# Kernel tuning notes

Measured on AMD Instinct MI355X. Metric: run time of the kernel, lower is better.

## Reference

```python
import jax, jax.numpy as jnp
import numpy as np

PROMPT_LEN = 2048
VOCAB = 49408
DIM = 768


def setup_inputs() -> dict:
    key = jax.random.key(0)
    k1, k2 = jax.random.split(key)
    # prompt_embs initialized ~ N(0, 0.02) per nn.init.normal_(std=0.02)
    prompt_embs = jax.random.normal(k1, (PROMPT_LEN, DIM), dtype=jnp.float32) * 0.02
    # codebook (CLIP embedding table), fixed data (not a trainable param)
    clip_embs = jax.random.normal(k2, (VOCAB, DIM), dtype=jnp.float32)
    return {"prompt_embs": prompt_embs, "clip_embs": clip_embs}


def _find_nearest(prompt_embs, clip_embs):
    # torch.cdist with p=2 -> Euclidean distance. argmin is invariant under sqrt,
    # so we use the expanded squared-distance form (single GEMM + norms),
    # avoiding materializing the [P, D]-broadcast difference tensor.
    p_sq = jnp.sum(prompt_embs * prompt_embs, axis=-1, keepdims=True)  # [P, 1]
    c_sq = jnp.sum(clip_embs * clip_embs, axis=-1)                      # [V]
    cross = jnp.einsum("pd,vd->pv", prompt_embs, clip_embs)            # [P, V]
    d2 = p_sq + c_sq[None, :] - 2.0 * cross                             # [P, V]
    return jnp.argmin(d2, axis=1)                                       # [P]


def reference(prompt_embs, clip_embs):
    prompt_ids = _find_nearest(prompt_embs, clip_embs)      # [P] int
    vocab_embs = clip_embs[prompt_ids, :]                   # [P, D] gather
    # straight-through: value = vocab_embs, gradient flows to prompt_embs
    out_embs = jax.lax.stop_gradient(vocab_embs - prompt_embs) + prompt_embs
    return out_embs, prompt_ids
```

## Files before the change

### kernel.cpp

```cpp
#include <hip/hip_runtime.h>
#include <float.h>

#define PROMPT_LEN 2048
#define VOCAB 49408
#define DIM 768
#define ROWS_TOTAL (VOCAB + PROMPT_LEN)
#define NS 16
#define TM 64
#define TN 32
#define KC 64
#define KQ (KC / 4)
#define EPS 0.008f


__global__ void __launch_bounds__(1024) k_sumsq(const float* __restrict__ prompt,
                                                const float* __restrict__ clip,
                                                float* __restrict__ csq,
                                                unsigned* __restrict__ scal) {
    int tid  = threadIdx.x;
    int wid  = tid >> 6;
    int lane = tid & 63;
    int base = blockIdx.x * 128 + wid * 8;

    if (blockIdx.x == 0 && tid == 0) scal[0] = 0u;

    float locMin = FLT_MAX, locMax = 0.f;
    for (int r = base; r < base + 8; r += 2) {
        const float* s0 = (r     < VOCAB) ? clip + (size_t)r * DIM
                                          : prompt + (size_t)(r - VOCAB) * DIM;
        const float* s1 = (r + 1 < VOCAB) ? clip + (size_t)(r + 1) * DIM
                                          : prompt + (size_t)(r + 1 - VOCAB) * DIM;
        float4 a0 = ((const float4*)s0)[lane];
        float4 a1 = ((const float4*)s0)[64 + lane];
        float4 a2 = ((const float4*)s0)[128 + lane];
        float4 b0 = ((const float4*)s1)[lane];
        float4 b1 = ((const float4*)s1)[64 + lane];
        float4 b2 = ((const float4*)s1)[128 + lane];
        float sA = a0.x*a0.x + a0.y*a0.y + a0.z*a0.z + a0.w*a0.w
                 + a1.x*a1.x + a1.y*a1.y + a1.z*a1.z + a1.w*a1.w
                 + a2.x*a2.x + a2.y*a2.y + a2.z*a2.z + a2.w*a2.w;
        float sB = b0.x*b0.x + b0.y*b0.y + b0.z*b0.z + b0.w*b0.w
                 + b1.x*b1.x + b1.y*b1.y + b1.z*b1.z + b1.w*b1.w
                 + b2.x*b2.x + b2.y*b2.y + b2.z*b2.z + b2.w*b2.w;
        #pragma unroll
        for (int m = 32; m >= 1; m >>= 1) {
            sA += __shfl_xor(sA, m, 64);
            sB += __shfl_xor(sB, m, 64);
        }
        if (r < VOCAB)     locMin = fminf(locMin, sA); else locMax = fmaxf(locMax, sA);
        if (r + 1 < VOCAB) locMin = fminf(locMin, sB); else locMax = fmaxf(locMax, sB);
        if (lane == 0) {
            if (r < VOCAB)     csq[r] = sA;
            if (r + 1 < VOCAB) csq[r + 1] = sB;
        }
    }
    __shared__ float smn[16], smx[16];
    if (lane == 0) { smn[wid] = locMin; smx[wid] = locMax; }
    __syncthreads();
    if (tid == 0) {
        float mn = FLT_MAX, mx = 0.f;
        #pragma unroll
        for (int w = 0; w < 16; ++w) { mn = fminf(mn, smn[w]); mx = fmaxf(mx, smx[w]); }
        atomicMin(&scal[1], __float_as_uint(mn));
        atomicMax((int*)&scal[2], (int)__float_as_uint(mx));
    }
}

__global__ void __launch_bounds__(256) k_compact(const float* __restrict__ csq,
                                                 int* __restrict__ cand,
                                                 unsigned* __restrict__ scal) {
    float cmin    = __uint_as_float(scal[1]);
    float pmax_sq = __uint_as_float(scal[2]);
    float B  = sqrtf(pmax_sq) * 1.0001f + 1e-6f;
    float U  = cmin + 2.f * B * sqrtf(cmin) + 1.0f;
    float sT = B + sqrtf(B * B + U);
    float T  = sT * sT;
    int v = blockIdx.x * 256 + threadIdx.x;
    if (v == 0) scal[3] = 0u;
    __shared__ int cnt, basep;
    if (threadIdx.x == 0) cnt = 0;
    __syncthreads();
    int keep = (v < VOCAB) && (csq[v] <= T);
    int pos = 0;
    if (keep) pos = atomicAdd(&cnt, 1);
    __syncthreads();
    if (threadIdx.x == 0 && cnt > 0) basep = atomicAdd((int*)&scal[0], cnt);
    __syncthreads();
    if (keep) cand[basep + pos] = v;
}

__global__ void __launch_bounds__(256, 4) k_score(const float* __restrict__ prompt,
                                                  const float* __restrict__ clip,
                                                  const float* __restrict__ csq,
                                                  const int* __restrict__ cand,
                                                  const unsigned* __restrict__ scal,
                                                  float* __restrict__ AB1,
                                                  float* __restrict__ AB2,
                                                  int* __restrict__ AIdx) {
    int mi = blockIdx.x / NS;
    int s  = blockIdx.x % NS;
    int m0 = mi * TM;
    int count  = (int)scal[0];
    int ntiles = (count + TN - 1) / TN;

    int tid = threadIdx.x;
    int mt = tid & 31;
    int nt = tid >> 5;

    __shared__ float Pl[TM][KC + 4];
    __shared__ float Cl[TN][KC + 4];
    __shared__ int   candS[TN];
    __shared__ float csqS[TN];
    __shared__ float mB1[TM][8], mB2[TM][8];
    __shared__ int   mBI[TM][8];

    float b1[2], b2[2]; int bi[2];
    #pragma unroll
    for (int j = 0; j < 2; ++j) { b1[j] = FLT_MAX; b2[j] = FLT_MAX; bi[j] = 0x7fffffff; }

    for (int tile = s; tile < ntiles; tile += NS) {
        __syncthreads();
        if (tid < TN) {
            int ci = tile * TN + tid;
            int v  = (ci < count) ? cand[ci] : 0;
            candS[tid] = v;
            csqS[tid]  = (ci < count) ? csq[v] : FLT_MAX;
        }
        __syncthreads();

        float acc[2][4];
        #pragma unroll
        for (int j = 0; j < 2; ++j)
            #pragma unroll
            for (int l = 0; l < 4; ++l) acc[j][l] = 0.f;

        for (int kc = 0; kc < DIM; kc += KC) {
            __syncthreads();
            #pragma unroll
            for (int f = 0; f < 4; ++f) {
                int j = tid + 256 * f;
                int r = j >> 4, c4 = j & 15;
                float4 v4 = *(const float4*)(prompt + (size_t)(m0 + r) * DIM + kc + c4 * 4);
                *(float4*)&Pl[r][c4 * 4] = v4;
            }
            #pragma unroll
            for (int f = 0; f < 2; ++f) {
                int j = tid + 256 * f;
                int n = j >> 4, c4 = j & 15;
                float4 v4 = *(const float4*)(clip + (size_t)candS[n] * DIM + kc + c4 * 4);
                *(float4*)&Cl[n][c4 * 4] = v4;
            }
            __syncthreads();
            #pragma unroll
            for (int q = 0; q < KQ; ++q) {
                float4 p[2], c[4];
                p[0] = *(const float4*)&Pl[mt][q * 4];
                p[1] = *(const float4*)&Pl[mt + 32][q * 4];
                #pragma unroll
                for (int l = 0; l < 4; ++l) c[l] = *(const float4*)&Cl[nt * 4 + l][q * 4];
                #pragma unroll
                for (int j = 0; j < 2; ++j)
                    #pragma unroll
                    for (int l = 0; l < 4; ++l) {
                        acc[j][l] = fmaf(p[j].x, c[l].x, acc[j][l]);
                        acc[j][l] = fmaf(p[j].y, c[l].y, acc[j][l]);
                        acc[j][l] = fmaf(p[j].z, c[l].z, acc[j][l]);
                        acc[j][l] = fmaf(p[j].w, c[l].w, acc[j][l]);
                    }
            }
        }

        #pragma unroll
        for (int l = 0; l < 4; ++l) {
            float cs = csqS[nt * 4 + l];
            if (cs < FLT_MAX) {
                int v = candS[nt * 4 + l];
                #pragma unroll
                for (int j = 0; j < 2; ++j) {
                    float d2 = fmaf(-2.f, acc[j][l], cs);
                    if (d2 < b1[j]) { b2[j] = b1[j]; b1[j] = d2; bi[j] = v; }
                    else if (d2 <= b2[j]) b2[j] = d2;
                }
            }
        }
    }

    __syncthreads();
    #pragma unroll
    for (int j = 0; j < 2; ++j) {
        mB1[mt + 32 * j][nt] = b1[j];
        mB2[mt + 32 * j][nt] = b2[j];
        mBI[mt + 32 * j][nt] = bi[j];
    }
    __syncthreads();
    if (tid < TM) {
        float B1 = FLT_MAX, B2 = FLT_MAX; int BI = 0x7fffffff;
        #pragma unroll
        for (int w = 0; w < 8; ++w) {
            float y1 = mB1[tid][w], y2 = mB2[tid][w]; int yi = mBI[tid][w];
            if (y1 < B1) { B2 = fminf(B1, y2); B1 = y1; BI = yi; }
            else         { B2 = fminf(B2, fminf(y1, y2)); }
        }
        int m = m0 + tid;
        AB1[m * NS + s] = B1;
        AB2[m * NS + s] = B2;
        AIdx[m * NS + s] = BI;
    }
}

__global__ void __launch_bounds__(256) k_merge(const float* __restrict__ prompt,
                                               const float* __restrict__ clip,
                                               const float* __restrict__ AB1,
                                               const float* __restrict__ AB2,
                                               const int* __restrict__ AIdx,
                                               unsigned* __restrict__ scal,
                                               int* __restrict__ amb,
                                               float* __restrict__ out) {
    int wid  = threadIdx.x >> 6;
    int lane = threadIdx.x & 63;
    int m = blockIdx.x * 4 + wid;
    int s = lane & 15;

    float b1 = AB1[m * NS + s];
    float b2 = AB2[m * NS + s];
    int   bi = AIdx[m * NS + s];
    #pragma unroll
    for (int msk = 1; msk <= 8; msk <<= 1) {
        float y1 = __shfl_xor(b1, msk, 64);
        float y2 = __shfl_xor(b2, msk, 64);
        int   yi = __shfl_xor(bi, msk, 64);
        if (y1 < b1) { b2 = fminf(b1, y2); b1 = y1; bi = yi; }
        else         { b2 = fminf(b2, fminf(y1, y2)); }
    }

    if (b2 - b1 < EPS) {
        if (lane == 0) {
            int pos = atomicAdd((int*)&scal[3], 1);
            amb[pos] = m;
        }
    } else {
        const float* crow = clip + (size_t)bi * DIM;
        const float* prow = prompt + (size_t)m * DIM;
        #pragma unroll
        for (int i = 0; i < 3; ++i) {
            float4 c = ((const float4*)crow)[i * 64 + lane];
            float4 p = ((const float4*)prow)[i * 64 + lane];
            float4 o;
            o.x = (c.x - p.x) + p.x;
            o.y = (c.y - p.y) + p.y;
            o.z = (c.z - p.z) + p.z;
            o.w = (c.w - p.w) + p.w;
            ((float4*)(out + (size_t)m * DIM))[i * 64 + lane] = o;
        }
        if (lane == 0) out[(size_t)PROMPT_LEN * DIM + m] = (float)bi;
    }
}

__global__ void __launch_bounds__(1024) k_fallback(const float* __restrict__ prompt,
                                                   const float* __restrict__ clip,
                                                   const int* __restrict__ cand,
                                                   const unsigned* __restrict__ scal,
                                                   const int* __restrict__ amb,
                                                   float* __restrict__ out) {
    int nAmb  = (int)scal[3];
    int count = (int)scal[0];
    int tid  = threadIdx.x;
    int wid  = tid >> 6;
    int lane = tid & 63;

    __shared__ double fB[16];
    __shared__ int    fI[16];
    __shared__ int    sWin;

    for (int a = blockIdx.x; a < nAmb; a += gridDim.x) {
        int m = amb[a];
        const float* prow = prompt + (size_t)m * DIM;
        double pd[12];
        #pragma unroll
        for (int i = 0; i < 3; ++i) {
            float4 v = ((const float4*)prow)[i * 64 + lane];
            pd[i*4+0] = (double)v.x; pd[i*4+1] = (double)v.y;
            pd[i*4+2] = (double)v.z; pd[i*4+3] = (double)v.w;
        }
        double best = 1e300;
        int bestIdx = 0x7fffffff;
        for (int ci = wid; ci < count; ci += 16) {
            int v = cand[ci];
            const float* crow = clip + (size_t)v * DIM;
            double sd = 0.0;
            #pragma unroll
            for (int i = 0; i < 3; ++i) {
                float4 c = ((const float4*)crow)[i * 64 + lane];
                double d0 = (double)c.x - pd[i*4+0];
                double d1 = (double)c.y - pd[i*4+1];
                double d2 = (double)c.z - pd[i*4+2];
                double d3 = (double)c.w - pd[i*4+3];
                sd = fma(d0, d0, sd); sd = fma(d1, d1, sd);
                sd = fma(d2, d2, sd); sd = fma(d3, d3, sd);
            }
            #pragma unroll
            for (int msk = 32; msk >= 1; msk >>= 1) sd += __shfl_xor(sd, msk, 64);
            if (sd < best || (sd == best && v < bestIdx)) { best = sd; bestIdx = v; }
        }
        if (lane == 0) { fB[wid] = best; fI[wid] = bestIdx; }
        __syncthreads();
        if (tid == 0) {
            double b = fB[0]; int bi2 = fI[0];
            #pragma unroll
            for (int w = 1; w < 16; ++w)
                if (fB[w] < b || (fB[w] == b && fI[w] < bi2)) { b = fB[w]; bi2 = fI[w]; }
            sWin = bi2;
        }
        __syncthreads();
        int win = sWin;

        if (tid < 192) {
            float4 c = ((const float4*)(clip + (size_t)win * DIM))[tid];
            float4 p = ((const float4*)prow)[tid];
            float4 o;
            o.x = (c.x - p.x) + p.x;
            o.y = (c.y - p.y) + p.y;
            o.z = (c.z - p.z) + p.z;
            o.w = (c.w - p.w) + p.w;
            ((float4*)(out + (size_t)m * DIM))[tid] = o;
        }
        if (tid == 0) out[(size_t)PROMPT_LEN * DIM + m] = (float)win;
        __syncthreads();
    }
}

extern "C" void kernel_launch(void* const* d_in, const int* in_sizes, int n_in,
                              void* d_out, int out_size, void* d_ws, size_t ws_size,
                              hipStream_t stream) {
    const float* prompt = (const float*)d_in[0];
    const float* clip   = (const float*)d_in[1];
    float* out = (float*)d_out;

    char* w = (char*)d_ws;
    float*    csq  = (float*)w;                    w += (size_t)VOCAB * 4;
    int*      cand = (int*)w;                      w += (size_t)VOCAB * 4;
    unsigned* scal = (unsigned*)w;                 w += 32;
    float*    AB1  = (float*)w;                    w += (size_t)PROMPT_LEN * NS * 4;
    float*    AB2  = (float*)w;                    w += (size_t)PROMPT_LEN * NS * 4;
    int*      AIdx = (int*)w;                      w += (size_t)PROMPT_LEN * NS * 4;
    int*      amb  = (int*)w;

    k_sumsq<<<ROWS_TOTAL / 128, 1024, 0, stream>>>(prompt, clip, csq, scal);
    k_compact<<<(VOCAB + 255) / 256, 256, 0, stream>>>(csq, cand, scal);
    k_score<<<(PROMPT_LEN / TM) * NS, 256, 0, stream>>>(prompt, clip, csq, cand, scal,
                                                        AB1, AB2, AIdx);
    k_merge<<<PROMPT_LEN / 4, 256, 0, stream>>>(prompt, clip, AB1, AB2, AIdx, scal, amb, out);
    k_fallback<<<128, 1024, 0, stream>>>(prompt, clip, cand, scal, amb, out);
}
```

Baseline: 358.2 us.

## Score candidates with split-bf16 MFMA matrix cores instead of fp32 FMA

Result: faster. 307.8 us (-14.1%).

```diff
diff --git a/kernel.cpp b/kernel.cpp
--- a/kernel.cpp
+++ b/kernel.cpp
@@ -5,13 +5,30 @@
 #define VOCAB 49408
 #define DIM 768
 #define ROWS_TOTAL (VOCAB + PROMPT_LEN)
-#define NS 16
-#define TM 64
-#define TN 32
-#define KC 64
-#define KQ (KC / 4)
+#define NS 32
+#define BM 64
+#define BN 64
+#define KCH 128
+#define NCHUNK (DIM / KCH)
+#define LDK (KCH + 8)
+#define CAND_MAX 4096
 #define EPS 0.008f
 
+typedef __attribute__((ext_vector_type(8))) short s8v;
+typedef __attribute__((ext_vector_type(4))) float fx4;
+
+
+__device__ inline unsigned short f2bf(float x) {
+    unsigned u = __float_as_uint(x);
+    u += 0x7FFFu + ((u >> 16) & 1u);
+    return (unsigned short)(u >> 16);
+}
+
+__device__ inline void merge2(float& b1, float& b2, int& bi,
+                              float y1, float y2, int yi) {
+    if (y1 < b1) { b2 = fminf(b1, y2); b1 = y1; bi = yi; }
+    else         { b2 = fminf(b2, fminf(y1, y2)); }
+}
 
 __global__ void __launch_bounds__(1024) k_sumsq(const float* __restrict__ prompt,
                                                 const float* __restrict__ clip,
@@ -89,121 +106,211 @@
     if (keep) cand[basep + pos] = v;
 }
 
-__global__ void __launch_bounds__(256, 4) k_score(const float* __restrict__ prompt,
-                                                  const float* __restrict__ clip,
-                                                  const float* __restrict__ csq,
-                                                  const int* __restrict__ cand,
-                                                  const unsigned* __restrict__ scal,
-                                                  float* __restrict__ AB1,
-                                                  float* __restrict__ AB2,
-                                                  int* __restrict__ AIdx) {
-    int mi = blockIdx.x / NS;
-    int s  = blockIdx.x % NS;
-    int m0 = mi * TM;
-    int count  = (int)scal[0];
-    int ntiles = (count + TN - 1) / TN;
-
-    int tid = threadIdx.x;
-    int mt = tid & 31;
-    int nt = tid >> 5;
-
-    __shared__ float Pl[TM][KC + 4];
-    __shared__ float Cl[TN][KC + 4];
-    __shared__ int   candS[TN];
-    __shared__ float csqS[TN];
-    __shared__ float mB1[TM][8], mB2[TM][8];
-    __shared__ int   mBI[TM][8];
-
-    float b1[2], b2[2]; int bi[2];
+__global__ void __launch_bounds__(256) k_convert(const float* __restrict__ prompt,
+                                                 const float* __restrict__ clip,
+                                                 const int* __restrict__ cand,
+                                                 const unsigned* __restrict__ scal,
+                                                 unsigned short* __restrict__ PbH,
+                                                 unsigned short* __restrict__ PbL,
+                                                 unsigned short* __restrict__ CbH,
+                                                 unsigned short* __restrict__ CbL) {
+    int count = (int)scal[0];
+    if (count > CAND_MAX) count = CAND_MAX;
+    int rows = PROMPT_LEN + count;
+    int wid  = threadIdx.x >> 6;
+    int lane = threadIdx.x & 63;
+    for (int r = blockIdx.x * 4 + wid; r < rows; r += gridDim.x * 4) {
+        const float* src;
+        unsigned short *dH, *dL;
+        if (r < PROMPT_LEN) {
+            src = prompt + (size_t)r * DIM;
+            dH = PbH + (size_t)r * DIM;  dL = PbL + (size_t)r * DIM;
+        } else {
+            int i = r - PROMPT_LEN;
+            src = clip + (size_t)cand[i] * DIM;
+            dH = CbH + (size_t)i * DIM;  dL = CbL + (size_t)i * DIM;
+        }
+        #pragma unroll
+        for (int i = 0; i < 3; ++i) {
+            float4 x = ((const float4*)src)[i * 64 + lane];
+            ushort4 h, l;
+            h.x = f2bf(x.x); l.x = f2bf(x.x - __uint_as_float((unsigned)h.x << 16));
+            h.y = f2bf(x.y); l.y = f2bf(x.y - __uint_as_float((unsigned)h.y << 16));
+            h.z = f2bf(x.z); l.z = f2bf(x.z - __uint_as_float((unsigned)h.z << 16));
+            h.w = f2bf(x.w); l.w = f2bf(x.w - __uint_as_float((unsigned)h.w << 16));
+            ((ushort4*)dH)[i * 64 + lane] = h;
+            ((ushort4*)dL)[i * 64 + lane] = l;
+        }
+    }
+}
+
+__global__ void __launch_bounds__(256, 2)
+k_score(const unsigned short* __restrict__ PbH, const unsigned short* __restrict__ PbL,
+        const unsigned short* __restrict__ CbH, const unsigned short* __restrict__ CbL,
+        const float* __restrict__ csq, const int* __restrict__ cand,
+        const unsigned* __restrict__ scal,
+        float* __restrict__ AB1, float* __restrict__ AB2, int* __restrict__ AIdx) {
+    int mi = blockIdx.x & 31;
+    int s  = blockIdx.x >> 5;
+    int m0 = mi * BM;
+    int count = (int)scal[0];
+    if (count > CAND_MAX) count = CAND_MAX;
+    int ntiles = (count + BN - 1) / BN;
+
+    int tid  = threadIdx.x;
+    int lane = tid & 63;
+    int wid  = tid >> 6;
+    int wr32 = (wid >> 1) * 32;
+    int wc32 = (wid & 1) * 32;
+    int l15  = lane & 15;
+    int l4   = lane >> 4;
+
+    __shared__ unsigned short Ah[BM][LDK], Al[BM][LDK];
+    __shared__ unsigned short Bh[BN][LDK], Bl[BN][LDK];
+    __shared__ int   candS[BN];
+    __shared__ float csqS[BN];
+    __shared__ float mB1[BM][2], mB2[BM][2];
+    __shared__ int   mBI[BM][2];
+
+    int srow[4], scol[4], offA[4];
     #pragma unroll
-    for (int j = 0; j < 2; ++j) { b1[j] = FLT_MAX; b2[j] = FLT_MAX; bi[j] = 0x7fffffff; }
+    for (int f = 0; f < 4; ++f) {
+        int j = tid + 256 * f;
+        srow[f] = j >> 4;
+        scol[f] = (j & 15) * 8;
+        offA[f] = (m0 + srow[f]) * DIM + scol[f];
+    }
+
+    float rb1[2][4], rb2[2][4]; int rbi[2][4];
+    #pragma unroll
+    for (int fm = 0; fm < 2; ++fm)
+        #pragma unroll
+        for (int j = 0; j < 4; ++j) { rb1[fm][j] = FLT_MAX; rb2[fm][j] = FLT_MAX; rbi[fm][j] = 0x7fffffff; }
 
     for (int tile = s; tile < ntiles; tile += NS) {
         __syncthreads();
-        if (tid < TN) {
-            int ci = tile * TN + tid;
+        if (tid < BN) {
+            int ci = tile * BN + tid;
             int v  = (ci < count) ? cand[ci] : 0;
             candS[tid] = v;
             csqS[tid]  = (ci < count) ? csq[v] : FLT_MAX;
         }
-        __syncthreads();
-
-        float acc[2][4];
-        #pragma unroll
-        for (int j = 0; j < 2; ++j)
-            #pragma unroll
-            for (int l = 0; l < 4; ++l) acc[j][l] = 0.f;
-
-        for (int kc = 0; kc < DIM; kc += KC) {
+
+        int offB[4];
+        #pragma unroll
+        for (int f = 0; f < 4; ++f) {
+            int rowc = tile * BN + srow[f];
+            if (rowc >= count) rowc = 0;
+            offB[f] = rowc * DIM + scol[f];
+        }
+
+        fx4 acc00 = {0.f,0.f,0.f,0.f}, acc01 = {0.f,0.f,0.f,0.f};
+        fx4 acc10 = {0.f,0.f,0.f,0.f}, acc11 = {0.f,0.f,0.f,0.f};
+
+        s8v rAh[4], rAl[4], rBh[4], rBl[4];
+        #pragma unroll
+        for (int f = 0; f < 4; ++f) {
+            rAh[f] = *(const s8v*)(PbH + offA[f]);
+            rAl[f] = *(const s8v*)(PbL + offA[f]);
+            rBh[f] = *(const s8v*)(CbH + offB[f]);
+            rBl[f] = *(const s8v*)(CbL + offB[f]);
+        }
+
+        #pragma unroll
+        for (int kc = 0; kc < NCHUNK; ++kc) {
             __syncthreads();
             #pragma unroll
             for (int f = 0; f < 4; ++f) {
-                int j = tid + 256 * f;
-                int r = j >> 4, c4 = j & 15;
-                float4 v4 = *(const float4*)(prompt + (size_t)(m0 + r) * DIM + kc + c4 * 4);
-                *(float4*)&Pl[r][c4 * 4] = v4;
-            }
-            #pragma unroll
-            for (int f = 0; f < 2; ++f) {
-                int j = tid + 256 * f;
-                int n = j >> 4, c4 = j & 15;
-                float4 v4 = *(const float4*)(clip + (size_t)candS[n] * DIM + kc + c4 * 4);
-                *(float4*)&Cl[n][c4 * 4] = v4;
+                *(s8v*)&Ah[srow[f]][scol[f]] = rAh[f];
+                *(s8v*)&Al[srow[f]][scol[f]] = rAl[f];
+                *(s8v*)&Bh[srow[f]][scol[f]] = rBh[f];
+                *(s8v*)&Bl[srow[f]][scol[f]] = rBl[f];
             }
             __syncthreads();
-            #pragma unroll
-            for (int q = 0; q < KQ; ++q) {
-                float4 p[2], c[4];
-                p[0] = *(const float4*)&Pl[mt][q * 4];
-                p[1] = *(const float4*)&Pl[mt + 32][q * 4];
+            if (kc + 1 < NCHUNK) {
+                int off = (kc + 1) * KCH;
                 #pragma unroll
-                for (int l = 0; l < 4; ++l) c[l] = *(const float4*)&Cl[nt * 4 + l][q * 4];
-                #pragma unroll
-                for (int j = 0; j < 2; ++j)
-                    #pragma unroll
-                    for (int l = 0; l < 4; ++l) {
-                        acc[j][l] = fmaf(p[j].x, c[l].x, acc[j][l]);
-                        acc[j][l] = fmaf(p[j].y, c[l].y, acc[j][l]);
-                        acc[j][l] = fmaf(p[j].z, c[l].z, acc[j][l]);
-                        acc[j][l] = fmaf(p[j].w, c[l].w, acc[j][l]);
-                    }
-            }
-        }
-
-        #pragma unroll
-        for (int l = 0; l < 4; ++l) {
-            float cs = csqS[nt * 4 + l];
-            if (cs < FLT_MAX) {
-                int v = candS[nt * 4 + l];
-                #pragma unroll
-                for (int j = 0; j < 2; ++j) {
-                    float d2 = fmaf(-2.f, acc[j][l], cs);
-                    if (d2 < b1[j]) { b2[j] = b1[j]; b1[j] = d2; bi[j] = v; }
-                    else if (d2 <= b2[j]) b2[j] = d2;
+                for (int f = 0; f < 4; ++f) {
+                    rAh[f] = *(const s8v*)(PbH + offA[f] + off);
+                    rAl[f] = *(const s8v*)(PbL + offA[f] + off);
+                    rBh[f] = *(const s8v*)(CbH + offB[f] + off);
+                    rBl[f] = *(const s8v*)(CbL + offB[f] + off);
                 }
             }
-        }
-    }
-
+            #pragma unroll
+            for (int kk = 0; kk < KCH / 32; ++kk) {
+                int ko = kk * 32 + l4 * 8;
+                s8v ah0 = *(const s8v*)&Ah[wr32      + l15][ko];
+                s8v ah1 = *(const s8v*)&Ah[wr32 + 16 + l15][ko];
+                s8v al0 = *(const s8v*)&Al[wr32      + l15][ko];
+                s8v al1 = *(const s8v*)&Al[wr32 + 16 + l15][ko];
+                s8v bh0 = *(const s8v*)&Bh[wc32      + l15][ko];
+                s8v bh1 = *(const s8v*)&Bh[wc32 + 16 + l15][ko];
+                s8v bl0 = *(const s8v*)&Bl[wc32      + l15][ko];
+                s8v bl1 = *(const s8v*)&Bl[wc32 + 16 + l15][ko];
+                acc00 = __builtin_amdgcn_mfma_f32_16x16x32_bf16(ah0, bh0, acc00, 0, 0, 0);
+                acc01 = __builtin_amdgcn_mfma_f32_16x16x32_bf16(ah0, bh1, acc01, 0, 0, 0);
+                acc10 = __builtin_amdgcn_mfma_f32_16x16x32_bf16(ah1, bh0, acc10, 0, 0, 0);
+                acc11 = __builtin_amdgcn_mfma_f32_16x16x32_bf16(ah1, bh1, acc11, 0, 0, 0);
+                acc00 = __builtin_amdgcn_mfma_f32_16x16x32_bf16(al0, bh0, acc00, 0, 0, 0);
+                acc01 = __builtin_amdgcn_mfma_f32_16x16x32_bf16(al0, bh1, acc01, 0, 0, 0);
+                acc10 = __builtin_amdgcn_mfma_f32_16x16x32_bf16(al1, bh0, acc10, 0, 0, 0);
+                acc11 = __builtin_amdgcn_mfma_f32_16x16x32_bf16(al1, bh1, acc11, 0, 0, 0);
+                acc00 = __builtin_amdgcn_mfma_f32_16x16x32_bf16(ah0, bl0, acc00, 0, 0, 0);
+                acc01 = __builtin_amdgcn_mfma_f32_16x16x32_bf16(ah0, bl1, acc01, 0, 0, 0);
+                acc10 = __builtin_amdgcn_mfma_f32_16x16x32_bf16(ah1, bl0, acc10, 0, 0, 0);
+                acc11 = __builtin_amdgcn_mfma_f32_16x16x32_bf16(ah1, bl1, acc11, 0, 0, 0);
+            }
+        }
+
+        float cs0 = csqS[wc32 + l15];       int v0 = candS[wc32 + l15];
+        float cs1 = csqS[wc32 + 16 + l15];  int v1 = candS[wc32 + 16 + l15];
+        #pragma unroll
+        for (int j = 0; j < 4; ++j) {
+            if (cs0 < FLT_MAX) {
+                float d2 = fmaf(-2.f, acc00[j], cs0);
+                if (d2 < rb1[0][j]) { rb2[0][j] = rb1[0][j]; rb1[0][j] = d2; rbi[0][j] = v0; }
+                else if (d2 <= rb2[0][j]) rb2[0][j] = d2;
+                d2 = fmaf(-2.f, acc10[j], cs0);
+                if (d2 < rb1[1][j]) { rb2[1][j] = rb1[1][j]; rb1[1][j] = d2; rbi[1][j] = v0; }
+                else if (d2 <= rb2[1][j]) rb2[1][j] = d2;
+            }
+            if (cs1 < FLT_MAX) {
+                float d2 = fmaf(-2.f, acc01[j], cs1);
+                if (d2 < rb1[0][j]) { rb2[0][j] = rb1[0][j]; rb1[0][j] = d2; rbi[0][j] = v1; }
+                else if (d2 <= rb2[0][j]) rb2[0][j] = d2;
+                d2 = fmaf(-2.f, acc11[j], cs1);
+                if (d2 < rb1[1][j]) { rb2[1][j] = rb1[1][j]; rb1[1][j] = d2; rbi[1][j] = v1; }
+                else if (d2 <= rb2[1][j]) rb2[1][j] = d2;
+            }
+        }
+    }
+
+    #pragma unroll
+    for (int fm = 0; fm < 2; ++fm)
+        #pragma unroll
+        for (int j = 0; j < 4; ++j) {
+            float b1 = rb1[fm][j], b2 = rb2[fm][j]; int bi = rbi[fm][j];
+            #pragma unroll
+            for (int msk = 1; msk <= 8; msk <<= 1) {
+                float y1 = __shfl_xor(b1, msk, 64);
+                float y2 = __shfl_xor(b2, msk, 64);
+                int   yi = __shfl_xor(bi, msk, 64);
+                merge2(b1, b2, bi, y1, y2, yi);
+            }
+            if (l15 == 0) {
+                int rl = wr32 + fm * 16 + l4 * 4 + j;
+                int wc = (wid & 1);
+                mB1[rl][wc] = b1; mB2[rl][wc] = b2; mBI[rl][wc] = bi;
+            }
+        }
     __syncthreads();
-    #pragma unroll
-    for (int j = 0; j < 2; ++j) {
-        mB1[mt + 32 * j][nt] = b1[j];
-        mB2[mt + 32 * j][nt] = b2[j];
-        mBI[mt + 32 * j][nt] = bi[j];
-    }
-    __syncthreads();
-    if (tid < TM) {
-        float B1 = FLT_MAX, B2 = FLT_MAX; int BI = 0x7fffffff;
-        #pragma unroll
-        for (int w = 0; w < 8; ++w) {
-            float y1 = mB1[tid][w], y2 = mB2[tid][w]; int yi = mBI[tid][w];
-            if (y1 < B1) { B2 = fminf(B1, y2); B1 = y1; BI = yi; }
-            else         { B2 = fminf(B2, fminf(y1, y2)); }
-        }
+    if (tid < BM) {
+        float B1 = mB1[tid][0], B2 = mB2[tid][0]; int BI = mBI[tid][0];
+        merge2(B1, B2, BI, mB1[tid][1], mB2[tid][1], mBI[tid][1]);
         int m = m0 + tid;
-        AB1[m * NS + s] = B1;
-        AB2[m * NS + s] = B2;
+        AB1[m * NS + s]  = B1;
+        AB2[m * NS + s]  = B2;
         AIdx[m * NS + s] = BI;
     }
 }
@@ -219,21 +326,21 @@
     int wid  = threadIdx.x >> 6;
     int lane = threadIdx.x & 63;
     int m = blockIdx.x * 4 + wid;
-    int s = lane & 15;
+    int s = lane & 31;
+    int count = (int)scal[0];
 
     float b1 = AB1[m * NS + s];
     float b2 = AB2[m * NS + s];
     int   bi = AIdx[m * NS + s];
     #pragma unroll
-    for (int msk = 1; msk <= 8; msk <<= 1) {
+    for (int msk = 1; msk <= 16; msk <<= 1) {
         float y1 = __shfl_xor(b1, msk, 64);
         float y2 = __shfl_xor(b2, msk, 64);
         int   yi = __shfl_xor(bi, msk, 64);
-        if (y1 < b1) { b2 = fminf(b1, y2); b1 = y1; bi = yi; }
-        else         { b2 = fminf(b2, fminf(y1, y2)); }
-    }
-
-    if (b2 - b1 < EPS) {
+        merge2(b1, b2, bi, y1, y2, yi);
+    }
+
+    if (count > CAND_MAX || b2 - b1 < EPS) {
         if (lane == 0) {
             int pos = atomicAdd((int*)&scal[3], 1);
             amb[pos] = m;
@@ -343,12 +450,17 @@
     float*    AB1  = (float*)w;                    w += (size_t)PROMPT_LEN * NS * 4;
     float*    AB2  = (float*)w;                    w += (size_t)PROMPT_LEN * NS * 4;
     int*      AIdx = (int*)w;                      w += (size_t)PROMPT_LEN * NS * 4;
-    int*      amb  = (int*)w;
+    int*      amb  = (int*)w;                      w += (size_t)PROMPT_LEN * 4;
+    unsigned short* PbH = (unsigned short*)w;      w += (size_t)PROMPT_LEN * DIM * 2;
+    unsigned short* PbL = (unsigned short*)w;      w += (size_t)PROMPT_LEN * DIM * 2;
+    unsigned short* CbH = (unsigned short*)w;      w += (size_t)CAND_MAX * DIM * 2;
+    unsigned short* CbL = (unsigned short*)w;      w += (size_t)CAND_MAX * DIM * 2;
 
     k_sumsq<<<ROWS_TOTAL / 128, 1024, 0, stream>>>(prompt, clip, csq, scal);
     k_compact<<<(VOCAB + 255) / 256, 256, 0, stream>>>(csq, cand, scal);
-    k_score<<<(PROMPT_LEN / TM) * NS, 256, 0, stream>>>(prompt, clip, csq, cand, scal,
-                                                        AB1, AB2, AIdx);
+    k_convert<<<1024, 256, 0, stream>>>(prompt, clip, cand, scal, PbH, PbL, CbH, CbL);
+    k_score<<<32 * NS, 256, 0, stream>>>(PbH, PbL, CbH, CbL, csq, cand, scal,
+                                         AB1, AB2, AIdx);
     k_merge<<<PROMPT_LEN / 4, 256, 0, stream>>>(prompt, clip, AB1, AB2, AIdx, scal, amb, out);
     k_fallback<<<128, 1024, 0, stream>>>(prompt, clip, cand, scal, amb, out);
 }
```
